# Performance work log

Measured on AMD Instinct MI355X. Metric: run time of the kernel, lower is better.

Reference implementation:

```python
import jax, jax.numpy as jnp
import numpy as np

B, IN, M = 64, 512, 1024

def setup_inputs() -> dict:
    key = jax.random.key(0)
    ks = jax.random.split(key, 20)
    inp = {
        'x': jax.random.normal(ks[0], (B, IN), jnp.float32),
        'h_prev': jax.random.normal(ks[1], (B, M), jnp.float32),
        'c_prev': jax.random.normal(ks[2], (B, M), jnp.float32),
        'C_prev': jax.random.normal(ks[3], (B, M, M), jnp.float32),
        'n_prev': jax.random.uniform(ks[4], (B, M), jnp.float32),
        'm_prev': jax.random.normal(ks[5], (B, M), jnp.float32),
    }
    # 6 Linear layers (weight [M, IN], bias [M]); small init so exp(Wi x) stays finite
    scale = 0.02
    names = ['q', 'k', 'v', 'i', 'f', 'o']
    for j, nm in enumerate(names):
        inp['W' + nm] = jax.random.normal(ks[6 + 2 * j], (M, IN), jnp.float32) * scale
        inp['b' + nm] = jax.random.normal(ks[7 + 2 * j], (M,), jnp.float32) * scale
    return inp


def reference(x, h_prev, c_prev, C_prev, n_prev, m_prev,
              Wq, bq, Wk, bk, Wv, bv, Wi, bi, Wf, bf, Wo, bo):
    mem = Wq.shape[0]
    q_t = x @ Wq.T + bq                                   # [B, M]
    k_t = (x @ Wk.T + bk) / jnp.sqrt(jnp.float32(mem))    # [B, M], 1/sqrt(M) scaling
    v_t = x @ Wv.T + bv                                   # [B, M]
    i_t = jnp.exp(x @ Wi.T + bi)                          # exponential input gate
    f_t = jax.nn.sigmoid(x @ Wf.T + bf)
    o_t = jax.nn.sigmoid(x @ Wo.T + bo)
    # rank-1 outer-product memory update: C_t[b] = diag(f)*C_prev + diag(i)*(v k^T)
    C_t = f_t[:, :, None] * C_prev + i_t[:, :, None] * (v_t[:, :, None] * k_t[:, None, :])
    n_t = f_t * n_prev + i_t * k_t
    h_tilde = jnp.einsum('bmn,bn->bm', C_t, q_t)          # matrix-vector read
    denom = jnp.maximum(jnp.einsum('bm,bm->b', n_t, q_t), 1.0)[:, None]
    h_t = o_t * (h_tilde / denom)
    # original returns (h_t, (h_t, c_prev, C_t, n_t, m_prev)); c_prev/m_prev are identity pass-through
    return h_t, C_t, n_t
```

## Files before the change

### kernel.cpp

```cpp
#include <hip/hip_runtime.h>
#include <math.h>

#define BATCH 64
#define IN_DIM 512
#define MEM 1024

typedef float f32x4 __attribute__((ext_vector_type(4)));

__global__ __launch_bounds__(256)
void gates_kernel(const float* __restrict__ x,
                  const float* __restrict__ Wq, const float* __restrict__ bq,
                  const float* __restrict__ Wk, const float* __restrict__ bk,
                  const float* __restrict__ Wv, const float* __restrict__ bv,
                  const float* __restrict__ Wi, const float* __restrict__ bi,
                  const float* __restrict__ Wf, const float* __restrict__ bf,
                  const float* __restrict__ Wo, const float* __restrict__ bo,
                  float* __restrict__ gates ) {
    __shared__ float xs[64][65];
    const int t    = threadIdx.x;
    const int lane = t & 63;
    const int wave = __builtin_amdgcn_readfirstlane(t >> 6);
    const int gm0  = blockIdx.x * 32 + wave * 8;
    const int g    = gm0 >> 10;
    const int m0   = gm0 & 1023;

    const float* W; const float* bias;
    switch (g) {
        case 0: W = Wq; bias = bq; break;
        case 1: W = Wk; bias = bk; break;
        case 2: W = Wv; bias = bv; break;
        case 3: W = Wi; bias = bi; break;
        case 4: W = Wf; bias = bf; break;
        default: W = Wo; bias = bo; break;
    }

    float acc[8];
#pragma unroll
    for (int j = 0; j < 8; ++j) acc[j] = 0.f;

    for (int kk = 0; kk < IN_DIM; kk += 64) {
        __syncthreads();
#pragma unroll
        for (int j = 0; j < 4; ++j) {
            int ii = t + j * 256;
            int bb = ii >> 4;
            int c4 = ii & 15;
            float4 v = *(const float4*)&x[bb * IN_DIM + kk + c4 * 4];
            xs[c4 * 4 + 0][bb] = v.x;
            xs[c4 * 4 + 1][bb] = v.y;
            xs[c4 * 4 + 2][bb] = v.z;
            xs[c4 * 4 + 3][bb] = v.w;
        }
        __syncthreads();

        const float* wp = W + (size_t)m0 * IN_DIM + kk;
#pragma unroll 2
        for (int k4 = 0; k4 < 16; ++k4) {
            float4 wv[8];
#pragma unroll
            for (int j = 0; j < 8; ++j)
                wv[j] = *(const float4*)(wp + j * IN_DIM + k4 * 4);
            float x0 = xs[k4 * 4 + 0][lane];
            float x1 = xs[k4 * 4 + 1][lane];
            float x2 = xs[k4 * 4 + 2][lane];
            float x3 = xs[k4 * 4 + 3][lane];
#pragma unroll
            for (int j = 0; j < 8; ++j) {
                acc[j] = fmaf(x0, wv[j].x, acc[j]);
                acc[j] = fmaf(x1, wv[j].y, acc[j]);
                acc[j] = fmaf(x2, wv[j].z, acc[j]);
                acc[j] = fmaf(x3, wv[j].w, acc[j]);
            }
        }
    }

    float v[8];
#pragma unroll
    for (int j = 0; j < 8; ++j) {
        float val = acc[j] + bias[m0 + j];
        if (g == 1)      val *= 0.03125f;
        else if (g == 3) val = __expf(val);
        else if (g >= 4) val = 1.f / (1.f + __expf(-val));
        v[j] = val;
    }
    float* outp = gates + (size_t)g * BATCH * MEM + (size_t)lane * MEM + m0;
    *(float4*)(outp + 0) = make_float4(v[0], v[1], v[2], v[3]);
    *(float4*)(outp + 4) = make_float4(v[4], v[5], v[6], v[7]);
}

__global__ __launch_bounds__(256)
void nt_denom_kernel(const float* __restrict__ gates,
                     const float* __restrict__ n_prev,
                     float* __restrict__ n_out,
                     float* __restrict__ denom) {
    const int b = blockIdx.x;
    const int t = threadIdx.x;
    const float* q  = gates + 0 * BATCH * MEM + (size_t)b * MEM;
    const float* k  = gates + 1 * BATCH * MEM + (size_t)b * MEM;
    const float* ig = gates + 3 * BATCH * MEM + (size_t)b * MEM;
    const float* fg = gates + 4 * BATCH * MEM + (size_t)b * MEM;

    float part = 0.f;
#pragma unroll
    for (int j = 0; j < 4; ++j) {
        int m = t + j * 256;
        float nt = fg[m] * n_prev[(size_t)b * MEM + m] + ig[m] * k[m];
        n_out[(size_t)b * MEM + m] = nt;
        part += nt * q[m];
    }
#pragma unroll
    for (int off = 32; off; off >>= 1) part += __shfl_xor(part, off, 64);

    __shared__ float red[4];
    if ((t & 63) == 0) red[t >> 6] = part;
    __syncthreads();
    if (t == 0) denom[b] = fmaxf(red[0] + red[1] + red[2] + red[3], 1.0f);
}

__global__ __launch_bounds__(256)
void update_kernel(const float* __restrict__ C_prev,
                   const float* __restrict__ gates,
                   const float* __restrict__ denom,
                   float* __restrict__ h_out,
                   float* __restrict__ C_out) {
    const int t    = threadIdx.x;
    const int wave = __builtin_amdgcn_readfirstlane(t >> 6);
    const int lane = t & 63;
    const int row0 = blockIdx.x * 16 + wave * 4;
    const int b    = row0 >> 10;
    const int m0   = row0 & 1023;

    const f32x4* qp = (const f32x4*)(gates + 0 * BATCH * MEM + (size_t)b * MEM);
    const f32x4* kp = (const f32x4*)(gates + 1 * BATCH * MEM + (size_t)b * MEM);

    f32x4 qv[4], kv[4];
#pragma unroll
    for (int c = 0; c < 4; ++c) {
        qv[c] = qp[c * 64 + lane];
        kv[c] = kp[c * 64 + lane];
    }

    float fm[4], iv[4], om[4];
#pragma unroll
    for (int r = 0; r < 4; ++r) {
        fm[r] = gates[4 * BATCH * MEM + (size_t)b * MEM + m0 + r];
        iv[r] = gates[3 * BATCH * MEM + (size_t)b * MEM + m0 + r] *
                gates[2 * BATCH * MEM + (size_t)b * MEM + m0 + r];
        om[r] = gates[5 * BATCH * MEM + (size_t)b * MEM + m0 + r];
    }
    const float inv_den = 1.0f / denom[b];

    f32x4 cv[4][4];
#pragma unroll
    for (int r = 0; r < 4; ++r) {
        const f32x4* cp = (const f32x4*)(C_prev + (size_t)(row0 + r) * MEM);
#pragma unroll
        for (int c = 0; c < 4; ++c)
            cv[r][c] = __builtin_nontemporal_load(&cp[c * 64 + lane]);
    }

    float acc[4];
#pragma unroll
    for (int r = 0; r < 4; ++r) {
        f32x4* co = (f32x4*)(C_out + (size_t)(row0 + r) * MEM);
        float a = 0.f;
#pragma unroll
        for (int c = 0; c < 4; ++c) {
            f32x4 ct;
            ct.x = fmaf(fm[r], cv[r][c].x, iv[r] * kv[c].x);
            ct.y = fmaf(fm[r], cv[r][c].y, iv[r] * kv[c].y);
            ct.z = fmaf(fm[r], cv[r][c].z, iv[r] * kv[c].z);
            ct.w = fmaf(fm[r], cv[r][c].w, iv[r] * kv[c].w);
            __builtin_nontemporal_store(ct, &co[c * 64 + lane]);
            a = fmaf(ct.x, qv[c].x, a);
            a = fmaf(ct.y, qv[c].y, a);
            a = fmaf(ct.z, qv[c].z, a);
            a = fmaf(ct.w, qv[c].w, a);
        }
        acc[r] = a;
    }

#pragma unroll
    for (int r = 0; r < 4; ++r)
#pragma unroll
        for (int off = 32; off; off >>= 1)
            acc[r] += __shfl_xor(acc[r], off, 64);

    if (lane == 0) {
#pragma unroll
        for (int r = 0; r < 4; ++r)
            h_out[row0 + r] = om[r] * acc[r] * inv_den;
    }
}

extern "C" void kernel_launch(void* const* d_in, const int* in_sizes, int n_in,
                              void* d_out, int out_size, void* d_ws, size_t ws_size,
                              hipStream_t stream) {
    const float* x      = (const float*)d_in[0];
    const float* C_prev = (const float*)d_in[3];
    const float* n_prev = (const float*)d_in[4];
    const float* Wq = (const float*)d_in[6];  const float* bq = (const float*)d_in[7];
    const float* Wk = (const float*)d_in[8];  const float* bk = (const float*)d_in[9];
    const float* Wv = (const float*)d_in[10]; const float* bv = (const float*)d_in[11];
    const float* Wi = (const float*)d_in[12]; const float* bi = (const float*)d_in[13];
    const float* Wf = (const float*)d_in[14]; const float* bf = (const float*)d_in[15];
    const float* Wo = (const float*)d_in[16]; const float* bo = (const float*)d_in[17];

    float* h_out = (float*)d_out;
    float* C_out = h_out + BATCH * MEM;
    float* n_out = C_out + (size_t)BATCH * MEM * MEM;

    float* gates = (float*)d_ws;
    float* denom = gates + 6 * BATCH * MEM;

    gates_kernel<<<192, 256, 0, stream>>>(x, Wq, bq, Wk, bk, Wv, bv,
                                          Wi, bi, Wf, bf, Wo, bo, gates);
    nt_denom_kernel<<<64, 256, 0, stream>>>(gates, n_prev, n_out, denom);
    update_kernel<<<4096, 256, 0, stream>>>(C_prev, gates, denom, h_out, C_out);
}
```

Measured before the change: 500.3 us.

## Fuse n_t and denominator computation into update kernel, drop nontemporal loads

Removes the separate nt_denom kernel launch by having every update block recompute n_t and the n·q dot product for its batch row, reducing it across waves through shared memory. Only one block per batch row writes n_out. This removes one launch and a dependency stage, but each of the 4096 blocks now does an extra 1024-element pass over n_prev and three gate vectors plus a block barrier. The C_prev loads also switch from nontemporal to regular loads.

```diff
diff --git a/kernel.cpp b/kernel.cpp
--- a/kernel.cpp
+++ b/kernel.cpp
@@ -89,40 +89,13 @@
 }
 
 __global__ __launch_bounds__(256)
-void nt_denom_kernel(const float* __restrict__ gates,
-                     const float* __restrict__ n_prev,
-                     float* __restrict__ n_out,
-                     float* __restrict__ denom) {
-    const int b = blockIdx.x;
-    const int t = threadIdx.x;
-    const float* q  = gates + 0 * BATCH * MEM + (size_t)b * MEM;
-    const float* k  = gates + 1 * BATCH * MEM + (size_t)b * MEM;
-    const float* ig = gates + 3 * BATCH * MEM + (size_t)b * MEM;
-    const float* fg = gates + 4 * BATCH * MEM + (size_t)b * MEM;
-
-    float part = 0.f;
-#pragma unroll
-    for (int j = 0; j < 4; ++j) {
-        int m = t + j * 256;
-        float nt = fg[m] * n_prev[(size_t)b * MEM + m] + ig[m] * k[m];
-        n_out[(size_t)b * MEM + m] = nt;
-        part += nt * q[m];
-    }
-#pragma unroll
-    for (int off = 32; off; off >>= 1) part += __shfl_xor(part, off, 64);
-
-    __shared__ float red[4];
-    if ((t & 63) == 0) red[t >> 6] = part;
-    __syncthreads();
-    if (t == 0) denom[b] = fmaxf(red[0] + red[1] + red[2] + red[3], 1.0f);
-}
-
-__global__ __launch_bounds__(256)
 void update_kernel(const float* __restrict__ C_prev,
                    const float* __restrict__ gates,
-                   const float* __restrict__ denom,
+                   const float* __restrict__ n_prev,
                    float* __restrict__ h_out,
-                   float* __restrict__ C_out) {
+                   float* __restrict__ C_out,
+                   float* __restrict__ n_out) {
+    __shared__ float red[4];
     const int t    = threadIdx.x;
     const int wave = __builtin_amdgcn_readfirstlane(t >> 6);
     const int lane = t & 63;
@@ -130,25 +103,27 @@
     const int b    = row0 >> 10;
     const int m0   = row0 & 1023;
 
-    const f32x4* qp = (const f32x4*)(gates + 0 * BATCH * MEM + (size_t)b * MEM);
-    const f32x4* kp = (const f32x4*)(gates + 1 * BATCH * MEM + (size_t)b * MEM);
+    const float* qb = gates + 0 * BATCH * MEM + (size_t)b * MEM;
+    const float* kb = gates + 1 * BATCH * MEM + (size_t)b * MEM;
+    const float* vb = gates + 2 * BATCH * MEM + (size_t)b * MEM;
+    const float* ib = gates + 3 * BATCH * MEM + (size_t)b * MEM;
+    const float* fb = gates + 4 * BATCH * MEM + (size_t)b * MEM;
+    const float* ob = gates + 5 * BATCH * MEM + (size_t)b * MEM;
 
     f32x4 qv[4], kv[4];
 #pragma unroll
     for (int c = 0; c < 4; ++c) {
-        qv[c] = qp[c * 64 + lane];
-        kv[c] = kp[c * 64 + lane];
+        qv[c] = ((const f32x4*)qb)[c * 64 + lane];
+        kv[c] = ((const f32x4*)kb)[c * 64 + lane];
     }
 
     float fm[4], iv[4], om[4];
 #pragma unroll
     for (int r = 0; r < 4; ++r) {
-        fm[r] = gates[4 * BATCH * MEM + (size_t)b * MEM + m0 + r];
-        iv[r] = gates[3 * BATCH * MEM + (size_t)b * MEM + m0 + r] *
-                gates[2 * BATCH * MEM + (size_t)b * MEM + m0 + r];
-        om[r] = gates[5 * BATCH * MEM + (size_t)b * MEM + m0 + r];
-    }
-    const float inv_den = 1.0f / denom[b];
+        fm[r] = fb[m0 + r];
+        iv[r] = ib[m0 + r] * vb[m0 + r];
+        om[r] = ob[m0 + r];
+    }
 
     f32x4 cv[4][4];
 #pragma unroll
@@ -156,7 +131,16 @@
         const f32x4* cp = (const f32x4*)(C_prev + (size_t)(row0 + r) * MEM);
 #pragma unroll
         for (int c = 0; c < 4; ++c)
-            cv[r][c] = __builtin_nontemporal_load(&cp[c * 64 + lane]);
+            cv[r][c] = cp[c * 64 + lane];
+    }
+
+    float ntv[4];
+    float dotp = 0.f;
+#pragma unroll
+    for (int j = 0; j < 4; ++j) {
+        int m = t + j * 256;
+        ntv[j] = fb[m] * n_prev[(size_t)b * MEM + m] + ib[m] * kb[m];
+        dotp += ntv[j] * qb[m];
     }
 
     float acc[4];
@@ -180,6 +164,19 @@
         acc[r] = a;
     }
 
+    if ((blockIdx.x & 63) == 0) {
+#pragma unroll
+        for (int j = 0; j < 4; ++j)
+            n_out[(size_t)b * MEM + t + j * 256] = ntv[j];
+    }
+
+#pragma unroll
+    for (int off = 32; off; off >>= 1) dotp += __shfl_xor(dotp, off, 64);
+    if (lane == 0) red[wave] = dotp;
+    __syncthreads();
+    const float denom = fmaxf(red[0] + red[1] + red[2] + red[3], 1.0f);
+    const float inv_den = 1.0f / denom;
+
 #pragma unroll
     for (int r = 0; r < 4; ++r)
 #pragma unroll
@@ -211,10 +208,9 @@
     float* n_out = C_out + (size_t)BATCH * MEM * MEM;
 
     float* gates = (float*)d_ws;
-    float* denom = gates + 6 * BATCH * MEM;
 
     gates_kernel<<<192, 256, 0, stream>>>(x, Wq, bq, Wk, bk, Wv, bv,
                                           Wi, bi, Wf, bf, Wo, bo, gates);
-    nt_denom_kernel<<<64, 256, 0, stream>>>(gates, n_prev, n_out, denom);
-    update_kernel<<<4096, 256, 0, stream>>>(C_prev, gates, denom, h_out, C_out);
+    update_kernel<<<4096, 256, 0, stream>>>(C_prev, gates, n_prev,
+                                            h_out, C_out, n_out);
 }
```

Result: slower. 530.9 us (+6.1%).

## Software-pipeline C row streaming in update kernel with fewer larger blocks

Applied to the files above, without the earlier changes.

The update kernel now gives each wave 16 rows instead of 4 and launches a quarter as many blocks. It walks the rows in pairs, prefetching the next row while computing the current one (double buffering in registers). Nontemporal loads and stores are replaced with ordinary ones. The goal is to amortize the per-block q/k loads and hide memory latency, at the cost of fewer blocks in flight and possibly more cache pollution.

```diff
diff --git a/kernel.cpp b/kernel.cpp
--- a/kernel.cpp
+++ b/kernel.cpp
@@ -123,73 +123,91 @@
                    const float* __restrict__ denom,
                    float* __restrict__ h_out,
                    float* __restrict__ C_out) {
-    const int t    = threadIdx.x;
-    const int wave = __builtin_amdgcn_readfirstlane(t >> 6);
-    const int lane = t & 63;
-    const int row0 = blockIdx.x * 16 + wave * 4;
-    const int b    = row0 >> 10;
-    const int m0   = row0 & 1023;
-
-    const f32x4* qp = (const f32x4*)(gates + 0 * BATCH * MEM + (size_t)b * MEM);
-    const f32x4* kp = (const f32x4*)(gates + 1 * BATCH * MEM + (size_t)b * MEM);
+    const int t     = threadIdx.x;
+    const int wave  = __builtin_amdgcn_readfirstlane(t >> 6);
+    const int lane  = t & 63;
+    const int wrow0 = blockIdx.x * 64 + wave * 16;
+    const int b     = blockIdx.x >> 4;
+    const int m0    = wrow0 & 1023;
+
+    const float* qb = gates + 0 * BATCH * MEM + (size_t)b * MEM;
+    const float* kb = gates + 1 * BATCH * MEM + (size_t)b * MEM;
+    const float* vb = gates + 2 * BATCH * MEM + (size_t)b * MEM;
+    const float* ib = gates + 3 * BATCH * MEM + (size_t)b * MEM;
+    const float* fb = gates + 4 * BATCH * MEM + (size_t)b * MEM;
+    const float* ob = gates + 5 * BATCH * MEM + (size_t)b * MEM;
 
     f32x4 qv[4], kv[4];
 #pragma unroll
     for (int c = 0; c < 4; ++c) {
-        qv[c] = qp[c * 64 + lane];
-        kv[c] = kp[c * 64 + lane];
-    }
-
-    float fm[4], iv[4], om[4];
-#pragma unroll
-    for (int r = 0; r < 4; ++r) {
-        fm[r] = gates[4 * BATCH * MEM + (size_t)b * MEM + m0 + r];
-        iv[r] = gates[3 * BATCH * MEM + (size_t)b * MEM + m0 + r] *
-                gates[2 * BATCH * MEM + (size_t)b * MEM + m0 + r];
-        om[r] = gates[5 * BATCH * MEM + (size_t)b * MEM + m0 + r];
+        qv[c] = ((const f32x4*)qb)[c * 64 + lane];
+        kv[c] = ((const f32x4*)kb)[c * 64 + lane];
     }
     const float inv_den = 1.0f / denom[b];
 
-    f32x4 cv[4][4];
-#pragma unroll
-    for (int r = 0; r < 4; ++r) {
-        const f32x4* cp = (const f32x4*)(C_prev + (size_t)(row0 + r) * MEM);
+    const f32x4* cp = (const f32x4*)(C_prev + (size_t)wrow0 * MEM);
+    f32x4*       co = (f32x4*)(C_out + (size_t)wrow0 * MEM);
+
+    f32x4 A[4], Bf[4];
+#pragma unroll
+    for (int c = 0; c < 4; ++c) A[c] = cp[c * 64 + lane];
+
+#pragma unroll 1
+    for (int rr = 0; rr < 16; rr += 2) {
+        const float fm0 = fb[m0 + rr],     iv0 = ib[m0 + rr] * vb[m0 + rr];
+        const float om0 = ob[m0 + rr];
+        const float fm1 = fb[m0 + rr + 1], iv1 = ib[m0 + rr + 1] * vb[m0 + rr + 1];
+        const float om1 = ob[m0 + rr + 1];
+
 #pragma unroll
         for (int c = 0; c < 4; ++c)
-            cv[r][c] = __builtin_nontemporal_load(&cp[c * 64 + lane]);
-    }
-
-    float acc[4];
-#pragma unroll
-    for (int r = 0; r < 4; ++r) {
-        f32x4* co = (f32x4*)(C_out + (size_t)(row0 + r) * MEM);
-        float a = 0.f;
+            Bf[c] = cp[(rr + 1) * 256 + c * 64 + lane];
+
+        float a0 = 0.f;
 #pragma unroll
         for (int c = 0; c < 4; ++c) {
             f32x4 ct;
-            ct.x = fmaf(fm[r], cv[r][c].x, iv[r] * kv[c].x);
-            ct.y = fmaf(fm[r], cv[r][c].y, iv[r] * kv[c].y);
-            ct.z = fmaf(fm[r], cv[r][c].z, iv[r] * kv[c].z);
-            ct.w = fmaf(fm[r], cv[r][c].w, iv[r] * kv[c].w);
-            __builtin_nontemporal_store(ct, &co[c * 64 + lane]);
-            a = fmaf(ct.x, qv[c].x, a);
-            a = fmaf(ct.y, qv[c].y, a);
-            a = fmaf(ct.z, qv[c].z, a);
-            a = fmaf(ct.w, qv[c].w, a);
-        }
-        acc[r] = a;
-    }
-
-#pragma unroll
-    for (int r = 0; r < 4; ++r)
-#pragma unroll
-        for (int off = 32; off; off >>= 1)
-            acc[r] += __shfl_xor(acc[r], off, 64);
-
-    if (lane == 0) {
-#pragma unroll
-        for (int r = 0; r < 4; ++r)
-            h_out[row0 + r] = om[r] * acc[r] * inv_den;
+            ct.x = fmaf(fm0, A[c].x, iv0 * kv[c].x);
+            ct.y = fmaf(fm0, A[c].y, iv0 * kv[c].y);
+            ct.z = fmaf(fm0, A[c].z, iv0 * kv[c].z);
+            ct.w = fmaf(fm0, A[c].w, iv0 * kv[c].w);
+            co[rr * 256 + c * 64 + lane] = ct;
+            a0 = fmaf(ct.x, qv[c].x, a0);
+            a0 = fmaf(ct.y, qv[c].y, a0);
+            a0 = fmaf(ct.z, qv[c].z, a0);
+            a0 = fmaf(ct.w, qv[c].w, a0);
+        }
+
+        if (rr + 2 < 16) {
+#pragma unroll
+            for (int c = 0; c < 4; ++c)
+                A[c] = cp[(rr + 2) * 256 + c * 64 + lane];
+        }
+
+        float a1 = 0.f;
+#pragma unroll
+        for (int c = 0; c < 4; ++c) {
+            f32x4 ct;
+            ct.x = fmaf(fm1, Bf[c].x, iv1 * kv[c].x);
+            ct.y = fmaf(fm1, Bf[c].y, iv1 * kv[c].y);
+            ct.z = fmaf(fm1, Bf[c].z, iv1 * kv[c].z);
+            ct.w = fmaf(fm1, Bf[c].w, iv1 * kv[c].w);
+            co[(rr + 1) * 256 + c * 64 + lane] = ct;
+            a1 = fmaf(ct.x, qv[c].x, a1);
+            a1 = fmaf(ct.y, qv[c].y, a1);
+            a1 = fmaf(ct.z, qv[c].z, a1);
+            a1 = fmaf(ct.w, qv[c].w, a1);
+        }
+
+#pragma unroll
+        for (int off = 32; off; off >>= 1) {
+            a0 += __shfl_xor(a0, off, 64);
+            a1 += __shfl_xor(a1, off, 64);
+        }
+        if (lane == 0) {
+            h_out[wrow0 + rr]     = om0 * a0 * inv_den;
+            h_out[wrow0 + rr + 1] = om1 * a1 * inv_den;
+        }
     }
 }
 
@@ -216,5 +234,5 @@
     gates_kernel<<<192, 256, 0, stream>>>(x, Wq, bq, Wk, bk, Wv, bv,
                                           Wi, bi, Wf, bf, Wo, bo, gates);
     nt_denom_kernel<<<64, 256, 0, stream>>>(gates, n_prev, n_out, denom);
-    update_kernel<<<4096, 256, 0, stream>>>(C_prev, gates, denom, h_out, C_out);
-}
+    update_kernel<<<1024, 256, 0, stream>>>(C_prev, gates, denom, h_out, C_out);
+}
```

Result: slower. 522.8 us (+4.5%).
